# Kernel tuning notes

Measured on AMD Instinct MI355X. Metric: run time of the kernel, lower is better.

## Reference

```python
import jax, jax.numpy as jnp
import numpy as np

SPATIAL = (14, 14)
FEATURE_DIM = 768
N, T, H, D = 16, 8, 12, 64
L = SPATIAL[0] * SPATIAL[1] + 1  # 197 (cls token + 196 patches)
W_SIZE = (2 * SPATIAL[0] - 1) * (2 * SPATIAL[1] - 1)  # 729


def _build_idx():
    # relative-position index map [196, 196], matches the torch double loop
    hs, ws = SPATIAL
    pos = np.arange(hs * ws)
    pi, pj = pos // ws, pos % ws
    i_offs = pi[:, None] - pi[None, :] + hs - 1
    j_offs = pj[:, None] - pj[None, :] + ws - 1
    return jnp.asarray(i_offs * (2 * ws - 1) + j_offs, dtype=jnp.int32)


def setup_inputs() -> dict:
    key = jax.random.key(0)
    kq, kk, kw1, kw2 = jax.random.split(key, 4)
    q = jax.random.normal(kq, (N, T, L, H, D), dtype=jnp.float32)
    k = jax.random.normal(kk, (N, T, L, H, D), dtype=jnp.float32)
    # learned relative-position bias tables (zeros in torch init; use small random for a meaningful baseline)
    w1 = jax.random.normal(kw1, (W_SIZE, FEATURE_DIM), dtype=jnp.float32) * 0.02
    w2 = jax.random.normal(kw2, (W_SIZE, FEATURE_DIM), dtype=jnp.float32) * 0.02
    idx = _build_idx()
    return {"q": q, "k": k, "w1": w1, "w2": w2, "idx": idx}


def _forward_half(q, k, w, idx):
    # q, k: [N, T', L, H, D]; strip cls token -> [N, T', 196, H, D]
    q = q[:, :, 1:]
    k = k[:, :, 1:]
    scale = 1.0 / jnp.sqrt(jnp.asarray(q.shape[-1], q.dtype))
    attn = jnp.einsum('ntqhd,ntkhd->ntqkh', q * scale, k)
    attn = jax.nn.softmax(attn, axis=-2).mean(axis=-1)  # [N, T', 196, 196]
    w_unroll = w[idx]  # gather: [196, 196, C]
    return jnp.einsum('ntqk,qkc->ntqc', attn, w_unroll)


def reference(q, k, w1, w2, idx):
    n, t, l, _, _ = q.shape
    c = w1.shape[-1]
    ret = jnp.zeros((n, t, l, c), dtype=q.dtype)
    ret = ret.at[:, 1:, 1:, :].add(_forward_half(q[:, 1:], k[:, :-1], w1, idx))
    ret = ret.at[:, :-1, 1:, :].add(_forward_half(q[:, :-1], k[:, 1:], w2, idx))
    return ret
```

## Files before the change

kernel.cpp:

```cpp
#include <hip/hip_runtime.h>

#define N_ 16
#define T_ 8
#define L_ 197
#define H_ 12
#define D_ 64
#define Q_ 196
#define C_ 768
#define KP 224
#define ENT 1792
#define ATS 216
#define APLANE 2112

typedef unsigned short ushort_t;
typedef __bf16 bf16x8 __attribute__((ext_vector_type(8)));
typedef float floatx4 __attribute__((ext_vector_type(4)));

#define GLD_LDS16(g, l)                                                    \
  __builtin_amdgcn_global_load_lds(                                        \
      (const __attribute__((address_space(1))) void*)(g),                  \
      (__attribute__((address_space(3))) void*)(l), 16, 0, 0)

static __device__ inline ushort_t f2bf(float x) {
  unsigned int u = __float_as_uint(x);
  u += 0x7fffu + ((u >> 16) & 1u);
  return (ushort_t)(u >> 16);
}
static __device__ inline unsigned int pack2(float a, float b) {
  return (unsigned int)f2bf(a) | ((unsigned int)f2bf(b) << 16);
}

__global__ __launch_bounds__(256) void convert_kernel(
    const float* __restrict__ q, const float* __restrict__ k,
    uint4* __restrict__ qb, uint4* __restrict__ kb) {
  const int nt  = blockIdx.x;
  const int pc  = blockIdx.y;
  const int inp = blockIdx.z;
  const int tid = threadIdx.x;
  const int pos0 = pc * 28;

  const float* src = inp ? k : q;
  const float sc = inp ? 1.f : 0.125f;
  uint4* dst = inp ? kb : qb;

  __shared__ uint2 lds[28][194];

  #pragma unroll
  for (int r = 0; r < 21; r++) {
    int e = tid + 256 * r;
    int row = e / 192, col = e - row * 192;
    float4 v = *(const float4*)(src + ((size_t)nt * L_ + 1 + pos0 + row) * (H_ * D_) + col * 4);
    uint2 p;
    p.x = pack2(v.x * sc, v.y * sc);
    p.y = pack2(v.z * sc, v.w * sc);
    lds[row][col] = p;
  }
  __syncthreads();

  #pragma unroll
  for (int r = 0; r < 11; r++) {
    int e = tid + 256 * r;
    if (e < 2688) {
      int hd = e / 28, p = e - hd * 28;
      uint2 a = lds[p][hd * 2];
      uint2 b = lds[p][hd * 2 + 1];
      int h = hd >> 3, dc = hd & 7;
      uint4 o; o.x = a.x; o.y = a.y; o.z = b.x; o.w = b.y;
      dst[((size_t)nt * H_ + h) * ENT + dc * KP + pos0 + p] = o;
    }
  }
}

__global__ __launch_bounds__(256, 2) void attn_kernel(
    const uint4* __restrict__ qb, const uint4* __restrict__ kb,
    ushort_t* __restrict__ A1, ushort_t* __restrict__ A2) {
  const int lin  = blockIdx.x;
  const int xcd  = lin & 7;
  const int slot = lin >> 3;
  const int g    = (slot >> 2) * 8 + xcd;
  const int b    = slot & 3;
  const int half = g / 112;
  const int nt   = g - half * 112;
  const int n  = nt / 7, tp = nt % 7;
  const int tq = (half == 0) ? tp + 1 : tp;
  const int tk = (half == 0) ? tp     : tp + 1;
  const int ntq = n * T_ + tq;
  const int ntk = n * T_ + tk;

  const uint4* qpl = qb + (size_t)ntq * H_ * ENT;
  const uint4* kpl = kb + (size_t)ntk * H_ * ENT;
  ushort_t* Ah = (half == 0) ? A1 : A2;

  __shared__ __align__(16) uint4 ks[2][ENT];
  ushort_t* at = (ushort_t*)ks;

  const int tid  = threadIdx.x;
  const int lane = tid & 63;
  const int wv   = tid >> 6;
  const int quad = lane >> 4;
  const int l15  = lane & 15;
  const int qi_b = 64 * b + 16 * wv;

  float accA[13][4];
  #pragma unroll
  for (int t = 0; t < 13; t++)
    #pragma unroll
    for (int r = 0; r < 4; r++) accA[t][r] = 0.f;

  auto stage = [&](int h, uint4* bufp) {
    #pragma unroll
    for (int r = 0; r < 7; r++)
      GLD_LDS16(kpl + (size_t)h * ENT + 256 * r + 64 * wv + lane,
                (char*)bufp + (256 * r + 64 * wv) * 16);
  };
  auto loadq = [&](int h, bf16x8* qf) {
    #pragma unroll
    for (int kk = 0; kk < 2; kk++)
      qf[kk] = *(const bf16x8*)&qpl[(size_t)h * ENT + (quad + 4 * kk) * KP + qi_b + l15];
  };

  auto headbody = [&](int h, uint4* bufp, bf16x8* qf, bool lastwait) {
    if (lastwait) asm volatile("s_waitcnt vmcnt(0)" ::: "memory");
    else          asm volatile("s_waitcnt vmcnt(9)" ::: "memory");
    __builtin_amdgcn_s_barrier();
    asm volatile("" ::: "memory");

    const ushort_t* bu = (const ushort_t*)bufp;
    floatx4 S[13];
    #pragma unroll
    for (int t = 0; t < 13; t++) S[t] = (floatx4){0.f, 0.f, 0.f, 0.f};
    #pragma unroll
    for (int kk = 0; kk < 2; kk++)
      #pragma unroll
      for (int t = 0; t < 13; t++) {
        bf16x8 bbv = *(const bf16x8*)&bu[((quad + 4 * kk) * KP + 16 * t + l15) * 8];
        S[t] = __builtin_amdgcn_mfma_f32_16x16x32_bf16(qf[kk], bbv, S[t], 0, 0, 0);
      }

    asm volatile("" ::: "memory");
    __builtin_amdgcn_s_barrier();
    if (h + 2 < H_) {
      loadq(h + 2, qf);
      stage(h + 2, bufp);
      __builtin_amdgcn_sched_barrier(0);
    }

    #pragma unroll
    for (int r = 0; r < 4; r++) {
      float s = 0.f;
      #pragma unroll
      for (int t = 0; t < 13; t++) {
        float e_ = (t == 12 && l15 >= 4) ? 0.f : __expf(S[t][r]);
        S[t][r] = e_;
        s += e_;
      }
      #pragma unroll
      for (int off = 1; off < 16; off <<= 1) s += __shfl_xor(s, off);
      float inv = 1.f / s;
      #pragma unroll
      for (int t = 0; t < 13; t++) accA[t][r] += S[t][r] * inv;
    }
  };

  bf16x8 qfA[2], qfB[2];
  loadq(0, qfA); stage(0, ks[0]);
  __builtin_amdgcn_sched_barrier(0);
  loadq(1, qfB); stage(1, ks[1]);
  __builtin_amdgcn_sched_barrier(0);

  #pragma unroll 1
  for (int hh = 0; hh < 6; hh++) {
    headbody(2 * hh,     ks[0], qfA, false);
    headbody(2 * hh + 1, ks[1], qfB, hh == 5);
  }

  const float s12 = 1.f / 12.f;
  #pragma unroll
  for (int t = 0; t < 13; t++)
    #pragma unroll
    for (int r = 0; r < 4; r++)
      at[(16 * wv + 4 * quad + r) * ATS + 16 * t + l15] = f2bf(accA[t][r] * s12);
  #pragma unroll
  for (int i = 0; i < 7; i++) {
    int e = lane + 64 * i;
    if (e < 416) {
      int row = e / 26, col = e - row * 26;
      uint4 v = *(const uint4*)&at[(16 * wv + row) * ATS + col * 8];
      int qi = qi_b + row;
      if (qi < Q_)
        *(uint4*)(Ah + ((size_t)qi * (N_ * T_) + ntq) * KP + col * 8) = v;
    }
  }
}

__global__ __launch_bounds__(256, 4) void mix_kernel(
    const ushort_t* __restrict__ A1, const ushort_t* __restrict__ A2,
    const float* __restrict__ w1, const float* __restrict__ w2,
    const int* __restrict__ idx, float* __restrict__ out) {
  const int ct = blockIdx.x;
  const int qi = blockIdx.y;
  const int tid  = threadIdx.x;
  const int lane = tid & 63;
  const int wv   = tid >> 6;
  const int quad = lane >> 4;
  const int l15  = lane & 15;
  const int p    = lane >> 2;
  const int cq   = lane & 3;

  __shared__ __align__(16) char As[2][4 * APLANE];
  __shared__ ushort_t Ws[128][40];

  int idxr0[7], idxr1[7];
  #pragma unroll
  for (int kc = 0; kc < 7; kc++) {
    int off = 32 * kc + 2 * p;
    if (off > 194) off = 194;
    int2 pr = *(const int2*)(idx + (size_t)qi * Q_ + off);
    idxr0[kc] = pr.x; idxr1[kc] = pr.y;
  }

  floatx4 acc[8][2];
  #pragma unroll
  for (int mt = 0; mt < 8; mt++)
    #pragma unroll
    for (int u = 0; u < 2; u++) acc[mt][u] = (floatx4){0.f, 0.f, 0.f, 0.f};

  float4 pw[2][2];
  const int cbase = ct * 128 + wv * 32;

  {
    const ushort_t* Ah_ = A1;
    #pragma unroll
    for (int r = 0; r < 2; r++)
      GLD_LDS16(Ah_ + ((size_t)qi * 128 + r * 64 + lane) * KP + wv * 8,
                As[0] + wv * APLANE + r * 1024);
    #pragma unroll
    for (int j = 0; j < 2; j++)
      #pragma unroll
      for (int u = 0; u < 2; u++)
        pw[j][u] = *(const float4*)(w1 + (size_t)(j ? idxr1[0] : idxr0[0]) * C_ +
                                    cbase + (cq + 4 * u) * 4);
  }

  #pragma unroll
  for (int ht = 0; ht < 14; ht++) {
    const int half = ht / 7, kc = ht % 7;
    __syncthreads();

    #pragma unroll
    for (int u = 0; u < 2; u++) {
      const float* f0 = (const float*)&pw[0][u];
      const float* f1 = (const float*)&pw[1][u];
      #pragma unroll
      for (int e = 0; e < 4; e++)
        *(unsigned int*)&Ws[wv * 32 + (cq + 4 * u) * 4 + e][2 * p] = pack2(f0[e], f1[e]);
    }

    if (ht + 1 < 14) {
      const int nh = (ht + 1) / 7, nk = (ht + 1) % 7;
      const ushort_t* Ah_ = nh ? A2 : A1;
      const float* w_ = nh ? w2 : w1;
      #pragma unroll
      for (int r = 0; r < 2; r++)
        GLD_LDS16(Ah_ + ((size_t)qi * 128 + r * 64 + lane) * KP + 32 * nk + wv * 8,
                  As[(ht + 1) & 1] + wv * APLANE + r * 1024);
      int r0 = idxr0[nk], r1 = idxr1[nk];
      #pragma unroll
      for (int u = 0; u < 2; u++) {
        pw[0][u] = *(const float4*)(w_ + (size_t)r0 * C_ + cbase + (cq + 4 * u) * 4);
        pw[1][u] = *(const float4*)(w_ + (size_t)r1 * C_ + cbase + (cq + 4 * u) * 4);
      }
    }

    const char* ab = As[ht & 1];
    bf16x8 bfv[2];
    #pragma unroll
    for (int u = 0; u < 2; u++)
      bfv[u] = *(const bf16x8*)&Ws[wv * 32 + 16 * u + l15][8 * quad];
    #pragma unroll
    for (int mt = 0; mt < 8; mt++) {
      bf16x8 a = *(const bf16x8*)(ab + quad * APLANE + (16 * mt + l15) * 16);
      acc[mt][0] = __builtin_amdgcn_mfma_f32_16x16x32_bf16(a, bfv[0], acc[mt][0], 0, 0, 0);
      acc[mt][1] = __builtin_amdgcn_mfma_f32_16x16x32_bf16(a, bfv[1], acc[mt][1], 0, 0, 0);
    }
  }

  #pragma unroll
  for (int u = 0; u < 2; u++) {
    const int c = ct * 128 + 32 * wv + 16 * u + l15;
    #pragma unroll
    for (int mt = 0; mt < 8; mt++)
      #pragma unroll
      for (int r = 0; r < 4; r++) {
        int m = 16 * mt + 4 * quad + r;
        out[((size_t)m * L_ + 1 + qi) * C_ + c] = acc[mt][u][r];
      }
  }
  if (qi == 0) {
    #pragma unroll
    for (int u = 0; u < 2; u++) {
      const int c = ct * 128 + 32 * wv + 16 * u + l15;
      #pragma unroll
      for (int mt = 0; mt < 8; mt++)
        #pragma unroll
        for (int r = 0; r < 4; r++) {
          int m = 16 * mt + 4 * quad + r;
          out[(size_t)m * L_ * C_ + c] = 0.f;
        }
    }
  }
}

extern "C" void kernel_launch(void* const* d_in, const int* in_sizes, int n_in,
                              void* d_out, int out_size, void* d_ws, size_t ws_size,
                              hipStream_t stream) {
  const float* q  = (const float*)d_in[0];
  const float* k  = (const float*)d_in[1];
  const float* w1 = (const float*)d_in[2];
  const float* w2 = (const float*)d_in[3];
  const int* idx  = (const int*)d_in[4];
  float* out = (float*)d_out;

  const size_t plane_tot = (size_t)(N_ * T_) * H_ * ENT;
  uint4* qb = (uint4*)d_ws;
  uint4* kb = qb + plane_tot;
  ushort_t* A1 = (ushort_t*)(kb + plane_tot);
  size_t Aelems = (size_t)Q_ * (N_ * T_) * KP;
  ushort_t* A2 = A1 + Aelems;

  hipMemsetAsync(A1, 0, Aelems * 2 * sizeof(ushort_t), stream);

  convert_kernel<<<dim3(N_ * T_, 7, 2), 256, 0, stream>>>(q, k, qb, kb);
  attn_kernel<<<dim3(896), 256, 0, stream>>>(qb, kb, A1, A2);
  mix_kernel<<<dim3(6, Q_), 256, 0, stream>>>(A1, A2, w1, w2, idx, out);
}
```

Measured before the change: 340.5 us.

## Restructure q/k bf16 conversion to one block per head with swizzled LDS

The fp32-to-bf16 convert kernel now assigns one block per (nt, head, input) instead of per 28-position chunk. Each thread loads 8 contiguous floats of one head's row and stores a packed uint4 into an XOR-swizzled LDS tile. It then writes the full 224-entry padded plane contiguously, zeroing the padding positions. The aim is fully coalesced contiguous output stores and fewer LDS bank conflicts, while the global reads become per-head strided 32-byte segments.

```diff
diff --git a/kernel.cpp b/kernel.cpp
--- a/kernel.cpp
+++ b/kernel.cpp
@@ -34,40 +34,44 @@
     const float* __restrict__ q, const float* __restrict__ k,
     uint4* __restrict__ qb, uint4* __restrict__ kb) {
   const int nt  = blockIdx.x;
-  const int pc  = blockIdx.y;
+  const int h   = blockIdx.y;
   const int inp = blockIdx.z;
   const int tid = threadIdx.x;
-  const int pos0 = pc * 28;
 
   const float* src = inp ? k : q;
   const float sc = inp ? 1.f : 0.125f;
-  uint4* dst = inp ? kb : qb;
-
-  __shared__ uint2 lds[28][194];
-
-  #pragma unroll
-  for (int r = 0; r < 21; r++) {
+  uint4* dst = (inp ? kb : qb) + ((size_t)nt * H_ + h) * ENT;
+
+  __shared__ __align__(16) uint4 lds[8 * KP];
+
+  const float* base = src + ((size_t)nt * L_ + 1) * (H_ * D_) + h * D_;
+
+  #pragma unroll
+  for (int r = 0; r < 7; r++) {
     int e = tid + 256 * r;
-    int row = e / 192, col = e - row * 192;
-    float4 v = *(const float4*)(src + ((size_t)nt * L_ + 1 + pos0 + row) * (H_ * D_) + col * 4);
-    uint2 p;
-    p.x = pack2(v.x * sc, v.y * sc);
-    p.y = pack2(v.z * sc, v.w * sc);
-    lds[row][col] = p;
+    if (e < 1568) {
+      int pos = e >> 3, dc = e & 7;
+      const float* p = base + (size_t)pos * (H_ * D_) + dc * 8;
+      float4 a  = *(const float4*)p;
+      float4 bv = *(const float4*)(p + 4);
+      uint4 o;
+      o.x = pack2(a.x * sc, a.y * sc);
+      o.y = pack2(a.z * sc, a.w * sc);
+      o.z = pack2(bv.x * sc, bv.y * sc);
+      o.w = pack2(bv.z * sc, bv.w * sc);
+      lds[dc * KP + ((pos & ~7) | ((pos ^ dc) & 7))] = o;
+    }
   }
   __syncthreads();
 
   #pragma unroll
-  for (int r = 0; r < 11; r++) {
+  for (int r = 0; r < 7; r++) {
     int e = tid + 256 * r;
-    if (e < 2688) {
-      int hd = e / 28, p = e - hd * 28;
-      uint2 a = lds[p][hd * 2];
-      uint2 b = lds[p][hd * 2 + 1];
-      int h = hd >> 3, dc = hd & 7;
-      uint4 o; o.x = a.x; o.y = a.y; o.z = b.x; o.w = b.y;
-      dst[((size_t)nt * H_ + h) * ENT + dc * KP + pos0 + p] = o;
-    }
+    int dc = e / KP, pos = e - dc * KP;
+    uint4 v;
+    if (pos < 196) v = lds[dc * KP + ((pos & ~7) | ((pos ^ dc) & 7))];
+    else           v = (uint4){0u, 0u, 0u, 0u};
+    dst[e] = v;
   }
 }
 
@@ -330,7 +334,7 @@
 
   hipMemsetAsync(A1, 0, Aelems * 2 * sizeof(ushort_t), stream);
 
-  convert_kernel<<<dim3(N_ * T_, 7, 2), 256, 0, stream>>>(q, k, qb, kb);
+  convert_kernel<<<dim3(N_ * T_, H_, 2), 256, 0, stream>>>(q, k, qb, kb);
   attn_kernel<<<dim3(896), 256, 0, stream>>>(qb, kb, A1, A2);
   mix_kernel<<<dim3(6, Q_), 256, 0, stream>>>(A1, A2, w1, w2, idx, out);
 }
```

Measured after the change: 338.3 us. Within noise of the previous version (-0.6%).
